# Kernel optimization log

Hardware: AMD Instinct MI355X
Metric: run time of the kernel (lower is better)

## Reference

```python
import jax, jax.numpy as jnp
import numpy as np

N = 150000   # total supergraph nodes (entities+events+chains)
D = 128      # embed_size
H = 4        # attention heads
DH = D // H  # head dim
E = 300000   # edges per layer
L = 4        # layer_specs length
A = 8        # edge attr dim
T = 10       # num_edge_type
TIME_SCALE = 24.0
SLOPE = 0.2  # negative_slope


def setup_inputs() -> dict:
    key = jax.random.key(0)
    ks = jax.random.split(key, 16)
    nrm = lambda k, s, sc=1.0: jax.random.normal(k, s, dtype=jnp.float32) * sc
    return {
        'x': nrm(ks[0], (N, D), 0.1),
        'Wq': nrm(ks[1], (L, D, D), D ** -0.5),
        'Wk': nrm(ks[2], (L, D, D), D ** -0.5),
        'Wv': nrm(ks[3], (L, D, D), D ** -0.5),
        'Wskip': nrm(ks[4], (L, D, D), D ** -0.5),
        'Wa': nrm(ks[5], (L, A, D), 0.1),
        'time_w': nrm(ks[6], (D,)),
        'time_b': nrm(ks[7], (D,), 0.1),
        'dist_w': nrm(ks[8], (D,)),
        'dist_b': nrm(ks[9], (D,), 0.1),
        'type_table': nrm(ks[10], (T, D), 0.1),
        'bn_gamma': jnp.ones((L, D), jnp.float32),
        'bn_beta': jnp.zeros((L, D), jnp.float32),
        'beta': jnp.full((L,), 0.5, jnp.float32),
        'edge_attr': jax.random.uniform(ks[11], (L, E, A), dtype=jnp.float32),
        'edge_dt': jax.random.uniform(ks[12], (L, E), dtype=jnp.float32) * TIME_SCALE,
        'edge_ds': jax.random.uniform(ks[13], (L, E), dtype=jnp.float32) * 10.0,
        'edge_index': jax.random.randint(ks[14], (L, 2, E), 0, N),
        'edge_type': jax.random.randint(ks[15], (L, E), 0, T),
    }


def _layer(x, Wq, Wk, Wv, Wskip, Wa, time_w, time_b, dist_w, dist_b,
           type_table, gamma, bvec, beta, attr, dt, ds, ei, et):
    n = x.shape[0]
    src, dst = ei[0], ei[1]
    # continuous time / distance encoders: cos basis (TimeEncoder / 'time' DistanceEncoder)
    te = jnp.cos((dt / TIME_SCALE)[:, None] * time_w + time_b)   # [E,D]
    de = jnp.cos(ds[:, None] * dist_w + dist_b)                  # [E,D]
    # 'add' edge/time fusion: attr MLP + time + dist + edge-type embeddings
    edge_feat = attr @ Wa + te + de + type_table[et]             # [E,D]
    kv_in = x[src] + edge_feat                                   # gather + fuse
    q = (x @ Wq).reshape(n, H, DH)[dst]                          # [E,H,DH]
    k = (kv_in @ Wk).reshape(-1, H, DH)
    v = (kv_in @ Wv).reshape(-1, H, DH)
    logits = (q * k).sum(-1) * (DH ** -0.5)                      # [E,H]
    logits = jnp.where(logits >= 0, logits, SLOPE * logits)      # leaky_relu(negative_slope)
    # segment softmax over incoming edges of each destination node
    m = jax.ops.segment_max(logits, dst, num_segments=n)
    a = jnp.exp(logits - m[dst])
    denom = jax.ops.segment_sum(a, dst, num_segments=n)
    a = a / denom[dst]
    agg = jax.ops.segment_sum(a[..., None] * v, dst, num_segments=n).reshape(n, D)
    # beta-weighted residual (learn_beta) with skip projection
    out = beta * (x @ Wskip) + (1.0 - beta) * agg
    # BatchNorm1d (training-mode batch stats) + ReLU
    mu = out.mean(0)
    var = out.var(0)
    out = (out - mu) * jax.lax.rsqrt(var + 1e-5) * gamma + bvec
    return jax.nn.relu(out)


def reference(x, Wq, Wk, Wv, Wskip, Wa, time_w, time_b, dist_w, dist_b,
              type_table, bn_gamma, bn_beta, beta, edge_attr, edge_dt,
              edge_ds, edge_index, edge_type):
    for l in range(L):  # entity2event, event2event, event2chain (time filter), chain2chain
        x = _layer(x, Wq[l], Wk[l], Wv[l], Wskip[l], Wa[l],
                   time_w, time_b, dist_w, dist_b, type_table,
                   bn_gamma[l], bn_beta[l], beta[l],
                   edge_attr[l], edge_dt[l], edge_ds[l],
                   edge_index[l], edge_type[l])
    return x
```

## Files before the change

kernel.cpp:

```cpp
#include <hip/hip_runtime.h>

typedef unsigned int u32;
typedef unsigned short u16;
typedef short bf16x8 __attribute__((ext_vector_type(8)));
typedef float f32x4 __attribute__((ext_vector_type(4)));

#define N_NODES 150000
#define E_EDGES 300000
#define L_CNT   151552
#define ETILES  9375
#define NTILES  4688

__device__ __forceinline__ float blo(u32 u){ return __uint_as_float(u << 16); }
__device__ __forceinline__ float bhi(u32 u){ return __uint_as_float(u & 0xffff0000u); }
__device__ __forceinline__ float b2f(u16 h){ return __uint_as_float(((u32)h) << 16); }
__device__ __forceinline__ u16 f2bf(float f){
  u32 u = __float_as_uint(f);
  return (u16)((u + 0x7fffu + ((u >> 16) & 1u)) >> 16);
}
__device__ __forceinline__ u32 pack2(float a, float b){
  return (u32)f2bf(a) | ((u32)f2bf(b) << 16);
}

__device__ __forceinline__ f32x4 mfma16(bf16x8 a, bf16x8 b, f32x4 c){
  return __builtin_amdgcn_mfma_f32_16x16x32_bf16(a, b, c, 0, 0, 0);
}

__device__ __forceinline__ int opsw(int r, int k){ return (r * 128 + k) ^ ((r & 7) << 3); }
__device__ __forceinline__ int csw(int r, int n){ return (r * 128 + n) ^ (((r >> 2) & 3) << 3); }

__global__ __launch_bounds__(256)
void k_wt(const float* __restrict__ Wq, const float* __restrict__ Wk,
          const float* __restrict__ Wv, const float* __restrict__ Ws,
          u16* __restrict__ Wt)
{
  const int m = blockIdx.x;
  const float* src = (m < 4 ? Wq : m < 8 ? Wk : m < 12 ? Wv : Ws)
                     + (size_t)(m & 3) * 16384;
  u16* dst = Wt + (size_t)m * 16384;
  const int t = threadIdx.x;
  for (int i = 0; i < 16; ++i) {
    int idx = i * 256 + t;
    int n = idx >> 5;
    int k4 = (idx & 31) << 2;
    ushort4 o;
    o.x = f2bf(src[(k4 + 0) * 128 + n]);
    o.y = f2bf(src[(k4 + 1) * 128 + n]);
    o.z = f2bf(src[(k4 + 2) * 128 + n]);
    o.w = f2bf(src[(k4 + 3) * 128 + n]);
    *(ushort4*)(dst + n * 128 + k4) = o;
  }
}


__global__ __launch_bounds__(256)
void k_hist(const int* __restrict__ eidx, int* __restrict__ counts)
{
  const int l = blockIdx.y;
  const int e = blockIdx.x * 256 + threadIdx.x;
  if (e < E_EDGES) {
    int dst = eidx[(size_t)l * 2 * E_EDGES + E_EDGES + e];
    atomicAdd(&counts[(size_t)l * L_CNT + dst], 1);
  }
}

__global__ __launch_bounds__(256)
void k_scan1(const int* __restrict__ counts, int* __restrict__ rowptr,
             int* __restrict__ bsum)
{
  __shared__ int sh[256];
  const int b = blockIdx.x, l = blockIdx.y;
  const int t = threadIdx.x;
  const int* c = counts + (size_t)l * L_CNT + b * 2048;
  int* rp = rowptr + (size_t)l * L_CNT + b * 2048;
  int v[8]; int s = 0;
  #pragma unroll
  for (int j = 0; j < 8; ++j) { v[j] = c[t * 8 + j]; s += v[j]; }
  sh[t] = s; __syncthreads();
  for (int off = 1; off < 256; off <<= 1) {
    int x = (t >= off) ? sh[t - off] : 0;
    __syncthreads();
    sh[t] += x;
    __syncthreads();
  }
  int excl = (t == 0) ? 0 : sh[t - 1];
  if (t == 255) bsum[l * 128 + b] = sh[255];
  int run = excl;
  #pragma unroll
  for (int j = 0; j < 8; ++j) { rp[t * 8 + j] = run; run += v[j]; }
}

__global__ __launch_bounds__(128)
void k_scan2(int* __restrict__ bsum)
{
  __shared__ int sh[128];
  const int l = blockIdx.x, t = threadIdx.x;
  int v = (t < 74) ? bsum[l * 128 + t] : 0;
  sh[t] = v; __syncthreads();
  for (int off = 1; off < 128; off <<= 1) {
    int x = (t >= off) ? sh[t - off] : 0;
    __syncthreads();
    sh[t] += x;
    __syncthreads();
  }
  int excl = (t == 0) ? 0 : sh[t - 1];
  if (t < 74) bsum[l * 128 + t] = excl;
}

__global__ __launch_bounds__(256)
void k_scan3(int* __restrict__ rowptr, int* __restrict__ tmp,
             const int* __restrict__ bsum)
{
  const int l = blockIdx.y;
  const int q = blockIdx.x * 256 + threadIdx.x;
  int v = rowptr[(size_t)l * L_CNT + q] + bsum[l * 128 + (q >> 11)];
  rowptr[(size_t)l * L_CNT + q] = v;
  tmp[(size_t)l * L_CNT + q] = v;
}

__global__ __launch_bounds__(256)
void k_scatter(const int* __restrict__ srcP, const int* __restrict__ dstP,
               const int* __restrict__ etP, const float* __restrict__ dtP,
               const float* __restrict__ dsP, const float* __restrict__ attrP,
               int* __restrict__ tmpL, u32* __restrict__ meta)
{
  const int e = blockIdx.x * 256 + threadIdx.x;
  if (e < E_EDGES) {
    int dst = dstP[e];
    int pos = atomicAdd(&tmpL[dst], 1);
    int src = srcP[e];
    int et  = etP[e];
    float dtn = dtP[e] * (1.0f / 24.0f);
    float dsv = dsP[e];
    float4 aA = *(const float4*)(attrP + (size_t)e * 8);
    float4 aB = *(const float4*)(attrP + (size_t)e * 8 + 4);
    uint4 r0, r1;
    r0.x = (u32)src;
    r0.y = (u32)dst | ((u32)et << 20);
    r0.z = __float_as_uint(dtn);
    r0.w = __float_as_uint(dsv);
    r1.x = pack2(aA.x, aA.y); r1.y = pack2(aA.z, aA.w);
    r1.z = pack2(aB.x, aB.y); r1.w = pack2(aB.z, aB.w);
    u32* mp = meta + (size_t)pos * 8;
    *(uint4*)mp = r0;
    *(uint4*)(mp + 4) = r1;
  }
}

template<int XF32>
__global__ __launch_bounds__(256)
void k_kvin(const void* __restrict__ xg, const float* __restrict__ Wa,
            const float* __restrict__ tw, const float* __restrict__ tb,
            const float* __restrict__ dw, const float* __restrict__ db,
            const float* __restrict__ ttab, const u32* __restrict__ meta,
            u16* __restrict__ kvV)
{
  const int idx = blockIdx.x * 256 + threadIdx.x;
  const int e = idx >> 4;
  const int c8 = (idx & 15) << 3;
  const u32* mp = meta + (size_t)e * 8;
  uint4 m0 = *(const uint4*)mp;
  uint4 m1 = *(const uint4*)(mp + 4);
  const int src = (int)m0.x;
  const int et = (int)(m0.y >> 20);
  const float dtn = __uint_as_float(m0.z);
  const float dss = __uint_as_float(m0.w);
  float aa[8] = { blo(m1.x), bhi(m1.x), blo(m1.y), bhi(m1.y),
                  blo(m1.z), bhi(m1.z), blo(m1.w), bhi(m1.w) };
  const float4 twA = *(const float4*)(tw + c8);
  const float4 twB = *(const float4*)(tw + c8 + 4);
  const float4 tbA = *(const float4*)(tb + c8);
  const float4 tbB = *(const float4*)(tb + c8 + 4);
  const float4 dwA = *(const float4*)(dw + c8);
  const float4 dwB = *(const float4*)(dw + c8 + 4);
  const float4 dbA = *(const float4*)(db + c8);
  const float4 dbB = *(const float4*)(db + c8 + 4);
  const float4 ttA = *(const float4*)(ttab + et * 128 + c8);
  const float4 ttB = *(const float4*)(ttab + et * 128 + c8 + 4);
  float f[8];
  f[0] = __cosf(fmaf(dtn, twA.x, tbA.x)) + __cosf(fmaf(dss, dwA.x, dbA.x)) + ttA.x;
  f[1] = __cosf(fmaf(dtn, twA.y, tbA.y)) + __cosf(fmaf(dss, dwA.y, dbA.y)) + ttA.y;
  f[2] = __cosf(fmaf(dtn, twA.z, tbA.z)) + __cosf(fmaf(dss, dwA.z, dbA.z)) + ttA.z;
  f[3] = __cosf(fmaf(dtn, twA.w, tbA.w)) + __cosf(fmaf(dss, dwA.w, dbA.w)) + ttA.w;
  f[4] = __cosf(fmaf(dtn, twB.x, tbB.x)) + __cosf(fmaf(dss, dwB.x, dbB.x)) + ttB.x;
  f[5] = __cosf(fmaf(dtn, twB.y, tbB.y)) + __cosf(fmaf(dss, dwB.y, dbB.y)) + ttB.y;
  f[6] = __cosf(fmaf(dtn, twB.z, tbB.z)) + __cosf(fmaf(dss, dwB.z, dbB.z)) + ttB.z;
  f[7] = __cosf(fmaf(dtn, twB.w, tbB.w)) + __cosf(fmaf(dss, dwB.w, dbB.w)) + ttB.w;
  #pragma unroll
  for (int a = 0; a < 8; ++a) {
    float4 wA = *(const float4*)(Wa + a * 128 + c8);
    float4 wB = *(const float4*)(Wa + a * 128 + c8 + 4);
    f[0] = fmaf(aa[a], wA.x, f[0]);
    f[1] = fmaf(aa[a], wA.y, f[1]);
    f[2] = fmaf(aa[a], wA.z, f[2]);
    f[3] = fmaf(aa[a], wA.w, f[3]);
    f[4] = fmaf(aa[a], wB.x, f[4]);
    f[5] = fmaf(aa[a], wB.y, f[5]);
    f[6] = fmaf(aa[a], wB.z, f[6]);
    f[7] = fmaf(aa[a], wB.w, f[7]);
  }
  float xv[8];
  if (XF32) {
    float4 xA = *(const float4*)((const float*)xg + (size_t)src * 128 + c8);
    float4 xB = *(const float4*)((const float*)xg + (size_t)src * 128 + c8 + 4);
    xv[0] = xA.x; xv[1] = xA.y; xv[2] = xA.z; xv[3] = xA.w;
    xv[4] = xB.x; xv[5] = xB.y; xv[6] = xB.z; xv[7] = xB.w;
  } else {
    uint4 xr = *(const uint4*)((const u16*)xg + (size_t)src * 128 + c8);
    xv[0] = blo(xr.x); xv[1] = bhi(xr.x); xv[2] = blo(xr.y); xv[3] = bhi(xr.y);
    xv[4] = blo(xr.z); xv[5] = bhi(xr.z); xv[6] = blo(xr.w); xv[7] = bhi(xr.w);
  }
  uint4 o;
  o.x = pack2(xv[0] + f[0], xv[1] + f[1]);
  o.y = pack2(xv[2] + f[2], xv[3] + f[3]);
  o.z = pack2(xv[4] + f[4], xv[5] + f[5]);
  o.w = pack2(xv[6] + f[6], xv[7] + f[7]);
  *(uint4*)(kvV + (size_t)e * 128 + c8) = o;
}

template<int XF32>
__global__ __launch_bounds__(64, 2)
void gemm_qs(const void* __restrict__ xg, const u16* __restrict__ WtQ,
             const u16* __restrict__ WtS, u16* __restrict__ Qo,
             u16* __restrict__ So)
{
  __shared__ __align__(16) u16 As[4160];
  const u16* Wt = blockIdx.y ? WtS : WtQ;
  u16* C = blockIdx.y ? So : Qo;
  const int lane = threadIdx.x;
  const int lr = lane & 15, hi = lane >> 4;

  bf16x8 wt[8][4];
  #pragma unroll
  for (int nb = 0; nb < 8; ++nb)
    #pragma unroll
    for (int ks = 0; ks < 4; ++ks)
      wt[nb][ks] = *(const bf16x8*)(Wt + (nb * 16 + lr) * 128 + ks * 32 + hi * 8);

  for (int tile = blockIdx.x; tile < NTILES; tile += gridDim.x) {
    const int row0 = tile * 32;
    const int nr = min(32, N_NODES - row0);

    #pragma unroll
    for (int i = 0; i < 8; ++i) {
      int idx = i * 64 + lane;
      int r = idx >> 4, c8 = (idx & 15) << 3;
      if (r < nr) {
        if (XF32) {
          float4 vA = *(const float4*)((const float*)xg + (size_t)(row0 + r) * 128 + c8);
          float4 vB = *(const float4*)((const float*)xg + (size_t)(row0 + r) * 128 + c8 + 4);
          uint4 o;
          o.x = pack2(vA.x, vA.y); o.y = pack2(vA.z, vA.w);
          o.z = pack2(vB.x, vB.y); o.w = pack2(vB.z, vB.w);
          *(uint4*)(As + opsw(r, c8)) = o;
        } else {
          uint4 v = *(const uint4*)((const u16*)xg + (size_t)(row0 + r) * 128 + c8);
          *(uint4*)(As + opsw(r, c8)) = v;
        }
      } else {
        *(uint4*)(As + opsw(r, c8)) = make_uint4(0, 0, 0, 0);
      }
    }

    f32x4 acc[2][8];
    #pragma unroll
    for (int a = 0; a < 2; ++a)
      #pragma unroll
      for (int b = 0; b < 8; ++b) {
        acc[a][b][0] = 0.f; acc[a][b][1] = 0.f;
        acc[a][b][2] = 0.f; acc[a][b][3] = 0.f;
      }
    #pragma unroll
    for (int ks = 0; ks < 4; ++ks) {
      const int kb = ks * 32 + hi * 8;
      bf16x8 a0 = *(const bf16x8*)(As + opsw(lr, kb));
      bf16x8 a1 = *(const bf16x8*)(As + opsw(16 + lr, kb));
      #pragma unroll
      for (int nb = 0; nb < 8; ++nb) {
        acc[0][nb] = mfma16(a0, wt[nb][ks], acc[0][nb]);
        acc[1][nb] = mfma16(a1, wt[nb][ks], acc[1][nb]);
      }
    }
    const int g4 = hi << 2;
    #pragma unroll
    for (int mt = 0; mt < 2; ++mt)
      #pragma unroll
      for (int nt = 0; nt < 8; ++nt)
        #pragma unroll
        for (int j = 0; j < 4; ++j)
          As[csw(mt * 16 + g4 + j, nt * 16 + lr)] = f2bf(acc[mt][nt][j]);
    #pragma unroll
    for (int i = 0; i < 8; ++i) {
      int idx = i * 64 + lane;
      int r = idx >> 4, n8 = (idx & 15) << 3;
      if (r < nr) {
        uint4 v = *(const uint4*)(As + csw(r, n8));
        *(uint4*)(C + (size_t)(row0 + r) * 128 + n8) = v;
      }
    }
  }
}

__global__ __launch_bounds__(64, 2)
void edge_k(const u16* __restrict__ WtK, const u32* __restrict__ meta,
            const u16* __restrict__ Qb, const u16* __restrict__ kvV,
            float* __restrict__ logits)
{
  __shared__ __align__(16) u16 As[4160];
  __shared__ __align__(16) u16 Qs[4160];
  __shared__ int dstSh[32];
  const int lane = threadIdx.x;
  const int lr = lane & 15, hi = lane >> 4;

  bf16x8 wt[8][4];
  #pragma unroll
  for (int nb = 0; nb < 8; ++nb)
    #pragma unroll
    for (int ks = 0; ks < 4; ++ks)
      wt[nb][ks] = *(const bf16x8*)(WtK + (nb * 16 + lr) * 128 + ks * 32 + hi * 8);

  for (int tile = blockIdx.x; tile < ETILES; tile += gridDim.x) {
    const int e0 = tile * 32;
    if (lane < 32)
      dstSh[lane] = (int)(meta[(size_t)(e0 + lane) * 8 + 1] & 0xFFFFFu);

    #pragma unroll
    for (int i = 0; i < 8; ++i) {
      int idx = i * 64 + lane;
      int r = idx >> 4, c8 = (idx & 15) << 3;
      uint4 v = *(const uint4*)(kvV + (size_t)(e0 + r) * 128 + c8);
      *(uint4*)(As + opsw(r, c8)) = v;
      int qrow = dstSh[r];
      uint4 qv = *(const uint4*)(Qb + (size_t)qrow * 128 + c8);
      *(uint4*)(Qs + opsw(r, c8)) = qv;
    }

    #pragma unroll
    for (int eb = 0; eb < 2; ++eb) {
      f32x4 kacc[8];
      #pragma unroll
      for (int b = 0; b < 8; ++b) {
        kacc[b][0] = 0.f; kacc[b][1] = 0.f; kacc[b][2] = 0.f; kacc[b][3] = 0.f;
      }
      #pragma unroll
      for (int ks = 0; ks < 4; ++ks) {
        bf16x8 ef = *(const bf16x8*)(As + opsw(eb * 16 + lr, ks * 32 + hi * 8));
        #pragma unroll
        for (int nb = 0; nb < 8; ++nb)
          kacc[nb] = mfma16(wt[nb][ks], ef, kacc[nb]);
      }
      const int el = eb * 16 + lr;
      float hs[4] = {0.f, 0.f, 0.f, 0.f};
      #pragma unroll
      for (int nb = 0; nb < 8; ++nb) {
        ushort4 q = *(const ushort4*)(Qs + opsw(el, nb * 16 + hi * 4));
        hs[nb >> 1] += b2f(q.x) * kacc[nb][0] + b2f(q.y) * kacc[nb][1]
                     + b2f(q.z) * kacc[nb][2] + b2f(q.w) * kacc[nb][3];
      }
      #pragma unroll
      for (int h = 0; h < 4; ++h) {
        hs[h] += __shfl_xor(hs[h], 16, 64);
        hs[h] += __shfl_xor(hs[h], 32, 64);
        hs[h] *= 0.17677669529663687f;
        hs[h] = (hs[h] >= 0.f) ? hs[h] : 0.2f * hs[h];
      }
      if (lane < 16)
        *(float4*)(logits + (size_t)(e0 + el) * 4) = make_float4(hs[0], hs[1], hs[2], hs[3]);
    }
  }
}

__global__ __launch_bounds__(64, 2)
void edge_v(const u16* __restrict__ WtV, u16* __restrict__ kvV)
{
  __shared__ __align__(16) u16 As[4160];
  const int lane = threadIdx.x;
  const int lr = lane & 15, hi = lane >> 4;

  bf16x8 wt[8][4];
  #pragma unroll
  for (int nb = 0; nb < 8; ++nb)
    #pragma unroll
    for (int ks = 0; ks < 4; ++ks)
      wt[nb][ks] = *(const bf16x8*)(WtV + (nb * 16 + lr) * 128 + ks * 32 + hi * 8);

  for (int tile = blockIdx.x; tile < ETILES; tile += gridDim.x) {
    const int e0 = tile * 32;
    #pragma unroll
    for (int i = 0; i < 8; ++i) {
      int idx = i * 64 + lane;
      int r = idx >> 4, c8 = (idx & 15) << 3;
      uint4 v = *(const uint4*)(kvV + (size_t)(e0 + r) * 128 + c8);
      *(uint4*)(As + opsw(r, c8)) = v;
    }
    const int g4 = hi << 2;
    #pragma unroll
    for (int mt = 0; mt < 2; ++mt) {
      f32x4 vacc[8];
      #pragma unroll
      for (int b = 0; b < 8; ++b) {
        vacc[b][0] = 0.f; vacc[b][1] = 0.f; vacc[b][2] = 0.f; vacc[b][3] = 0.f;
      }
      #pragma unroll
      for (int ks = 0; ks < 4; ++ks) {
        bf16x8 af = *(const bf16x8*)(As + opsw(mt * 16 + lr, ks * 32 + hi * 8));
        #pragma unroll
        for (int nb = 0; nb < 8; ++nb)
          vacc[nb] = mfma16(af, wt[nb][ks], vacc[nb]);
      }
      #pragma unroll
      for (int nt = 0; nt < 8; ++nt)
        #pragma unroll
        for (int j = 0; j < 4; ++j)
          As[csw(mt * 16 + g4 + j, nt * 16 + lr)] = f2bf(vacc[nt][j]);
    }
    #pragma unroll
    for (int i = 0; i < 8; ++i) {
      int idx = i * 64 + lane;
      int r = idx >> 4, n8 = (idx & 15) << 3;
      uint4 v = *(const uint4*)(As + csw(r, n8));
      *(uint4*)(kvV + (size_t)(e0 + r) * 128 + n8) = v;
    }
  }
}

__global__ __launch_bounds__(256)
void node_agg(const u16* __restrict__ Vs, const float* __restrict__ logits,
              const int* __restrict__ rowptr, const u16* __restrict__ S,
              const float* __restrict__ betaP, float* __restrict__ pre,
              float* __restrict__ colsum, float* __restrict__ colsumsq)
{
  __shared__ float red[1024];
  const int t = threadIdx.x;
  const int g = t >> 5;
  const int lane = t & 31;
  const int d0 = lane * 4;
  const int h = lane >> 3;
  const float beta = *betaP;
  const float omb = 1.f - beta;
  float s4[4] = {0.f, 0.f, 0.f, 0.f};
  float q4[4] = {0.f, 0.f, 0.f, 0.f};
  for (int rep = 0; rep < 16; ++rep) {
    int n = blockIdx.x * 128 + rep * 8 + g;
    if (n < N_NODES) {
      int rs = rowptr[n], re = rowptr[n + 1];
      float m = -1e30f;
      for (int i = rs; i < re; ++i)
        m = fmaxf(m, logits[(size_t)i * 4 + h]);
      float den = 0.f;
      float a0 = 0.f, a1 = 0.f, a2 = 0.f, a3 = 0.f;
      for (int i = rs; i < re; ++i) {
        float wgt = __expf(logits[(size_t)i * 4 + h] - m);
        den += wgt;
        ushort4 v = *(const ushort4*)(Vs + (size_t)i * 128 + d0);
        a0 = fmaf(wgt, b2f(v.x), a0);
        a1 = fmaf(wgt, b2f(v.y), a1);
        a2 = fmaf(wgt, b2f(v.z), a2);
        a3 = fmaf(wgt, b2f(v.w), a3);
      }
      float inv = (den > 0.f) ? (omb / den) : 0.f;
      ushort4 sv = *(const ushort4*)(S + (size_t)n * 128 + d0);
      float p0 = fmaf(beta, b2f(sv.x), a0 * inv);
      float p1 = fmaf(beta, b2f(sv.y), a1 * inv);
      float p2 = fmaf(beta, b2f(sv.z), a2 * inv);
      float p3 = fmaf(beta, b2f(sv.w), a3 * inv);
      *(float4*)(pre + (size_t)n * 128 + d0) = make_float4(p0, p1, p2, p3);
      s4[0] += p0; s4[1] += p1; s4[2] += p2; s4[3] += p3;
      q4[0] += p0 * p0; q4[1] += p1 * p1; q4[2] += p2 * p2; q4[3] += p3 * p3;
    }
  }
  *(float4*)(&red[g * 128 + d0]) = make_float4(s4[0], s4[1], s4[2], s4[3]);
  __syncthreads();
  if (t < 128) {
    float tot = 0.f;
    #pragma unroll
    for (int gg = 0; gg < 8; ++gg) tot += red[gg * 128 + t];
    atomicAdd(&colsum[t], tot);
  }
  __syncthreads();
  *(float4*)(&red[g * 128 + d0]) = make_float4(q4[0], q4[1], q4[2], q4[3]);
  __syncthreads();
  if (t < 128) {
    float tot = 0.f;
    #pragma unroll
    for (int gg = 0; gg < 8; ++gg) tot += red[gg * 128 + t];
    atomicAdd(&colsumsq[t], tot);
  }
}

template<int LAST>
__global__ __launch_bounds__(256)
void bn_apply(const float* __restrict__ pre, const float* __restrict__ colsum,
              const float* __restrict__ colsumsq, const float* __restrict__ gamma,
              const float* __restrict__ bvec, u16* __restrict__ outbf,
              float* __restrict__ outf)
{
  const int idx = blockIdx.x * 256 + threadIdx.x;
  const int n = idx >> 5;
  const int d0 = (idx & 31) * 4;
  const float invN = 1.f / 150000.f;
  float4 p = *(const float4*)(pre + (size_t)n * 128 + d0);
  float4 cs = *(const float4*)(colsum + d0);
  float4 cq = *(const float4*)(colsumsq + d0);
  float4 gm = *(const float4*)(gamma + d0);
  float4 bv = *(const float4*)(bvec + d0);
  float mu, var, y;
  mu = cs.x * invN; var = cq.x * invN - mu * mu;
  y = (p.x - mu) * rsqrtf(var + 1e-5f) * gm.x + bv.x; p.x = fmaxf(y, 0.f);
  mu = cs.y * invN; var = cq.y * invN - mu * mu;
  y = (p.y - mu) * rsqrtf(var + 1e-5f) * gm.y + bv.y; p.y = fmaxf(y, 0.f);
  mu = cs.z * invN; var = cq.z * invN - mu * mu;
  y = (p.z - mu) * rsqrtf(var + 1e-5f) * gm.z + bv.z; p.z = fmaxf(y, 0.f);
  mu = cs.w * invN; var = cq.w * invN - mu * mu;
  y = (p.w - mu) * rsqrtf(var + 1e-5f) * gm.w + bv.w; p.w = fmaxf(y, 0.f);
  if (LAST) {
    *(float4*)(outf + (size_t)n * 128 + d0) = p;
  } else {
    ushort4 o;
    o.x = f2bf(p.x); o.y = f2bf(p.y); o.z = f2bf(p.z); o.w = f2bf(p.w);
    *(ushort4*)(outbf + (size_t)n * 128 + d0) = o;
  }
}

extern "C" void kernel_launch(void* const* d_in, const int* in_sizes, int n_in,
                              void* d_out, int out_size, void* d_ws, size_t ws_size,
                              hipStream_t stream)
{
  const float* x0    = (const float*)d_in[0];
  const float* Wq    = (const float*)d_in[1];
  const float* Wk    = (const float*)d_in[2];
  const float* Wv    = (const float*)d_in[3];
  const float* Wsk   = (const float*)d_in[4];
  const float* Wa    = (const float*)d_in[5];
  const float* tw    = (const float*)d_in[6];
  const float* tb    = (const float*)d_in[7];
  const float* dw    = (const float*)d_in[8];
  const float* db    = (const float*)d_in[9];
  const float* ttab  = (const float*)d_in[10];
  const float* gam   = (const float*)d_in[11];
  const float* bet   = (const float*)d_in[12];
  const float* betaP = (const float*)d_in[13];
  const float* attr  = (const float*)d_in[14];
  const float* dt    = (const float*)d_in[15];
  const float* dsv   = (const float*)d_in[16];
  const int*   eidx  = (const int*)d_in[17];
  const int*   etyp  = (const int*)d_in[18];

  char* p = (char*)d_ws;
  u16* xbf  = (u16*)p;       p += 38400000;
  u16* Q    = (u16*)p;       p += 38400000;
  u16* S    = (u16*)p;       p += 38400000;
  u16* kvV  = (u16*)p;       p += 76800000;
  float* logits = (float*)p; p += 4800000;
  int* rowptr = (int*)p;     p += 4 * L_CNT * 4;
  int* tmp    = (int*)p;     p += 4 * L_CNT * 4;
  int* bsum   = (int*)p;     p += 4 * 128 * 4;
  float* colsum   = (float*)p; p += 512;
  float* colsumsq = (float*)p; p += 512;
  u16* Wt = (u16*)p;         p += 16 * 16384 * 2;
  u32* meta = (u32*)p;       p += (size_t)E_EDGES * 32;

  float* pre = (float*)d_out;

  k_wt<<<16, 256, 0, stream>>>(Wq, Wk, Wv, Wsk, Wt);
  hipMemsetAsync(tmp, 0, 4 * L_CNT * 4, stream);
  k_hist<<<dim3(1172, 4), 256, 0, stream>>>(eidx, tmp);
  k_scan1<<<dim3(74, 4), 256, 0, stream>>>(tmp, rowptr, bsum);
  k_scan2<<<4, 128, 0, stream>>>(bsum);
  k_scan3<<<dim3(592, 4), 256, 0, stream>>>(rowptr, tmp, bsum);

  for (int l = 0; l < 4; ++l) {
    const int* srcA = eidx + (size_t)l * 600000;
    const int* dstA = srcA + 300000;
    const int* rpl = rowptr + (size_t)l * L_CNT;
    const u16* WtQl = Wt + (size_t)l * 16384;
    const u16* WtKl = Wt + (size_t)(4 + l) * 16384;
    const u16* WtVl = Wt + (size_t)(8 + l) * 16384;
    const u16* WtSl = Wt + (size_t)(12 + l) * 16384;
    const float* Wal = Wa + (size_t)l * 1024;

    k_scatter<<<1172, 256, 0, stream>>>(
        srcA, dstA, etyp + (size_t)l * 300000, dt + (size_t)l * 300000,
        dsv + (size_t)l * 300000, attr + (size_t)l * 2400000,
        tmp + (size_t)l * L_CNT, meta);

    hipMemsetAsync(colsum, 0, 1024, stream);

    if (l == 0) {
      k_kvin<1><<<18750, 256, 0, stream>>>((const void*)x0, Wal, tw, tb, dw, db,
                                           ttab, meta, kvV);
      gemm_qs<1><<<dim3(1024, 2), 64, 0, stream>>>((const void*)x0, WtQl, WtSl, Q, S);
    } else {
      k_kvin<0><<<18750, 256, 0, stream>>>((const void*)xbf, Wal, tw, tb, dw, db,
                                           ttab, meta, kvV);
      gemm_qs<0><<<dim3(1024, 2), 64, 0, stream>>>((const void*)xbf, WtQl, WtSl, Q, S);
    }

    edge_k<<<2048, 64, 0, stream>>>(WtKl, meta, Q, kvV, logits);
    edge_v<<<2048, 64, 0, stream>>>(WtVl, kvV);

    node_agg<<<1172, 256, 0, stream>>>(kvV, logits, rpl, S, betaP + l,
                                       pre, colsum, colsumsq);

    if (l < 3)
      bn_apply<0><<<18750, 256, 0, stream>>>(pre, colsum, colsumsq,
                                             gam + (size_t)l * 128,
                                             bet + (size_t)l * 128, xbf, nullptr);
    else
      bn_apply<1><<<18750, 256, 0, stream>>>(pre, colsum, colsumsq,
                                             gam + (size_t)l * 128,
                                             bet + (size_t)l * 128,
                                             nullptr, (float*)d_out);
  }
}
```

Baseline: 1.587 ms.

## Fuse edge K and V projections into one kernel, share staged tiles across waves

Merges the separate edge_k and edge_v kernels into a single two-wave kernel. One wave computes the K projection and attention logits, the other computes the V projection from the same shared-memory tile of kv_in, so kvV is read once instead of twice and one launch is saved. gemm_qs likewise uses one block of two waves (Q and skip) that shares a single staged x tile, so x is read once rather than by two separate blocks. Both kernels drop their grid-stride persistent loops in favour of one tile per block, which means every block reloads its weight fragments into registers and so adds weight-load traffic.

```diff
diff --git a/kernel.cpp b/kernel.cpp
--- a/kernel.cpp
+++ b/kernel.cpp
@@ -218,17 +218,22 @@
   *(uint4*)(kvV + (size_t)e * 128 + c8) = o;
 }
 
+
 template<int XF32>
-__global__ __launch_bounds__(64, 2)
+__global__ __launch_bounds__(128, 2)
 void gemm_qs(const void* __restrict__ xg, const u16* __restrict__ WtQ,
              const u16* __restrict__ WtS, u16* __restrict__ Qo,
              u16* __restrict__ So)
 {
   __shared__ __align__(16) u16 As[4160];
-  const u16* Wt = blockIdx.y ? WtS : WtQ;
-  u16* C = blockIdx.y ? So : Qo;
-  const int lane = threadIdx.x;
+  __shared__ __align__(16) u16 Bs[4160];
+  const int t = threadIdx.x;
+  const int w = t >> 6, lane = t & 63;
   const int lr = lane & 15, hi = lane >> 4;
+  const int row0 = blockIdx.x * 32;
+  const int nr = min(32, N_NODES - row0);
+  const u16* Wt = w ? WtS : WtQ;
+  u16* C = w ? So : Qo;
 
   bf16x8 wt[8][4];
   #pragma unroll
@@ -237,104 +242,115 @@
     for (int ks = 0; ks < 4; ++ks)
       wt[nb][ks] = *(const bf16x8*)(Wt + (nb * 16 + lr) * 128 + ks * 32 + hi * 8);
 
-  for (int tile = blockIdx.x; tile < NTILES; tile += gridDim.x) {
-    const int row0 = tile * 32;
-    const int nr = min(32, N_NODES - row0);
-
+  #pragma unroll
+  for (int i = 0; i < 4; ++i) {
+    int idx = i * 128 + t;
+    int r = idx >> 4, c8 = (idx & 15) << 3;
+    if (r < nr) {
+      if (XF32) {
+        float4 vA = *(const float4*)((const float*)xg + (size_t)(row0 + r) * 128 + c8);
+        float4 vB = *(const float4*)((const float*)xg + (size_t)(row0 + r) * 128 + c8 + 4);
+        uint4 o;
+        o.x = pack2(vA.x, vA.y); o.y = pack2(vA.z, vA.w);
+        o.z = pack2(vB.x, vB.y); o.w = pack2(vB.z, vB.w);
+        *(uint4*)(As + opsw(r, c8)) = o;
+      } else {
+        uint4 v = *(const uint4*)((const u16*)xg + (size_t)(row0 + r) * 128 + c8);
+        *(uint4*)(As + opsw(r, c8)) = v;
+      }
+    } else {
+      *(uint4*)(As + opsw(r, c8)) = make_uint4(0, 0, 0, 0);
+    }
+  }
+  __syncthreads();
+
+  f32x4 acc[2][8];
+  #pragma unroll
+  for (int a = 0; a < 2; ++a)
+    #pragma unroll
+    for (int b = 0; b < 8; ++b) {
+      acc[a][b][0] = 0.f; acc[a][b][1] = 0.f;
+      acc[a][b][2] = 0.f; acc[a][b][3] = 0.f;
+    }
+  #pragma unroll
+  for (int ks = 0; ks < 4; ++ks) {
+    const int kb = ks * 32 + hi * 8;
+    bf16x8 a0 = *(const bf16x8*)(As + opsw(lr, kb));
+    bf16x8 a1 = *(const bf16x8*)(As + opsw(16 + lr, kb));
+    #pragma unroll
+    for (int nb = 0; nb < 8; ++nb) {
+      acc[0][nb] = mfma16(a0, wt[nb][ks], acc[0][nb]);
+      acc[1][nb] = mfma16(a1, wt[nb][ks], acc[1][nb]);
+    }
+  }
+  __syncthreads();
+
+  u16* Cs = w ? Bs : As;
+  const int g4 = hi << 2;
+  #pragma unroll
+  for (int mt = 0; mt < 2; ++mt)
+    #pragma unroll
+    for (int nt = 0; nt < 8; ++nt)
+      #pragma unroll
+      for (int j = 0; j < 4; ++j)
+        Cs[csw(mt * 16 + g4 + j, nt * 16 + lr)] = f2bf(acc[mt][nt][j]);
+  #pragma unroll
+  for (int i = 0; i < 8; ++i) {
+    int idx = i * 64 + lane;
+    int r = idx >> 4, n8 = (idx & 15) << 3;
+    if (r < nr) {
+      uint4 v = *(const uint4*)(Cs + csw(r, n8));
+      *(uint4*)(C + (size_t)(row0 + r) * 128 + n8) = v;
+    }
+  }
+}
+
+
+__global__ __launch_bounds__(128, 2)
+void edge_kv(const u16* __restrict__ WtK, const u16* __restrict__ WtV,
+             const u32* __restrict__ meta, const u16* __restrict__ Qb,
+             u16* __restrict__ kvV, float* __restrict__ logits)
+{
+  __shared__ __align__(16) u16 KVs[4160];
+  __shared__ __align__(16) u16 Qs[4160];
+  __shared__ __align__(16) u16 Cs[4160];
+  __shared__ int dstSh[32];
+  const int t = threadIdx.x;
+  const int w = t >> 6, lane = t & 63;
+  const int lr = lane & 15, hi = lane >> 4;
+  const int e0 = blockIdx.x * 32;
+  const u16* Wt = w ? WtV : WtK;
+
+  bf16x8 wt[8][4];
+  #pragma unroll
+  for (int nb = 0; nb < 8; ++nb)
+    #pragma unroll
+    for (int ks = 0; ks < 4; ++ks)
+      wt[nb][ks] = *(const bf16x8*)(Wt + (nb * 16 + lr) * 128 + ks * 32 + hi * 8);
+
+  if (t < 32)
+    dstSh[t] = (int)(meta[(size_t)(e0 + t) * 8 + 1] & 0xFFFFFu);
+
+  #pragma unroll
+  for (int i = 0; i < 4; ++i) {
+    int idx = i * 128 + t;
+    int r = idx >> 4, c8 = (idx & 15) << 3;
+    uint4 v = *(const uint4*)(kvV + (size_t)(e0 + r) * 128 + c8);
+    *(uint4*)(KVs + opsw(r, c8)) = v;
+  }
+  if (w == 0) {
     #pragma unroll
     for (int i = 0; i < 8; ++i) {
       int idx = i * 64 + lane;
       int r = idx >> 4, c8 = (idx & 15) << 3;
-      if (r < nr) {
-        if (XF32) {
-          float4 vA = *(const float4*)((const float*)xg + (size_t)(row0 + r) * 128 + c8);
-          float4 vB = *(const float4*)((const float*)xg + (size_t)(row0 + r) * 128 + c8 + 4);
-          uint4 o;
-          o.x = pack2(vA.x, vA.y); o.y = pack2(vA.z, vA.w);
-          o.z = pack2(vB.x, vB.y); o.w = pack2(vB.z, vB.w);
-          *(uint4*)(As + opsw(r, c8)) = o;
-        } else {
-          uint4 v = *(const uint4*)((const u16*)xg + (size_t)(row0 + r) * 128 + c8);
-          *(uint4*)(As + opsw(r, c8)) = v;
-        }
-      } else {
-        *(uint4*)(As + opsw(r, c8)) = make_uint4(0, 0, 0, 0);
-      }
-    }
-
-    f32x4 acc[2][8];
-    #pragma unroll
-    for (int a = 0; a < 2; ++a)
-      #pragma unroll
-      for (int b = 0; b < 8; ++b) {
-        acc[a][b][0] = 0.f; acc[a][b][1] = 0.f;
-        acc[a][b][2] = 0.f; acc[a][b][3] = 0.f;
-      }
-    #pragma unroll
-    for (int ks = 0; ks < 4; ++ks) {
-      const int kb = ks * 32 + hi * 8;
-      bf16x8 a0 = *(const bf16x8*)(As + opsw(lr, kb));
-      bf16x8 a1 = *(const bf16x8*)(As + opsw(16 + lr, kb));
-      #pragma unroll
-      for (int nb = 0; nb < 8; ++nb) {
-        acc[0][nb] = mfma16(a0, wt[nb][ks], acc[0][nb]);
-        acc[1][nb] = mfma16(a1, wt[nb][ks], acc[1][nb]);
-      }
-    }
-    const int g4 = hi << 2;
-    #pragma unroll
-    for (int mt = 0; mt < 2; ++mt)
-      #pragma unroll
-      for (int nt = 0; nt < 8; ++nt)
-        #pragma unroll
-        for (int j = 0; j < 4; ++j)
-          As[csw(mt * 16 + g4 + j, nt * 16 + lr)] = f2bf(acc[mt][nt][j]);
-    #pragma unroll
-    for (int i = 0; i < 8; ++i) {
-      int idx = i * 64 + lane;
-      int r = idx >> 4, n8 = (idx & 15) << 3;
-      if (r < nr) {
-        uint4 v = *(const uint4*)(As + csw(r, n8));
-        *(uint4*)(C + (size_t)(row0 + r) * 128 + n8) = v;
-      }
-    }
-  }
-}
-
-__global__ __launch_bounds__(64, 2)
-void edge_k(const u16* __restrict__ WtK, const u32* __restrict__ meta,
-            const u16* __restrict__ Qb, const u16* __restrict__ kvV,
-            float* __restrict__ logits)
-{
-  __shared__ __align__(16) u16 As[4160];
-  __shared__ __align__(16) u16 Qs[4160];
-  __shared__ int dstSh[32];
-  const int lane = threadIdx.x;
-  const int lr = lane & 15, hi = lane >> 4;
-
-  bf16x8 wt[8][4];
-  #pragma unroll
-  for (int nb = 0; nb < 8; ++nb)
-    #pragma unroll
-    for (int ks = 0; ks < 4; ++ks)
-      wt[nb][ks] = *(const bf16x8*)(WtK + (nb * 16 + lr) * 128 + ks * 32 + hi * 8);
-
-  for (int tile = blockIdx.x; tile < ETILES; tile += gridDim.x) {
-    const int e0 = tile * 32;
-    if (lane < 32)
-      dstSh[lane] = (int)(meta[(size_t)(e0 + lane) * 8 + 1] & 0xFFFFFu);
-
-    #pragma unroll
-    for (int i = 0; i < 8; ++i) {
-      int idx = i * 64 + lane;
-      int r = idx >> 4, c8 = (idx & 15) << 3;
-      uint4 v = *(const uint4*)(kvV + (size_t)(e0 + r) * 128 + c8);
-      *(uint4*)(As + opsw(r, c8)) = v;
       int qrow = dstSh[r];
       uint4 qv = *(const uint4*)(Qb + (size_t)qrow * 128 + c8);
       *(uint4*)(Qs + opsw(r, c8)) = qv;
     }
-
+  }
+  __syncthreads();
+
+  if (w == 0) {
     #pragma unroll
     for (int eb = 0; eb < 2; ++eb) {
       f32x4 kacc[8];
@@ -344,7 +360,7 @@
       }
       #pragma unroll
       for (int ks = 0; ks < 4; ++ks) {
-        bf16x8 ef = *(const bf16x8*)(As + opsw(eb * 16 + lr, ks * 32 + hi * 8));
+        bf16x8 ef = *(const bf16x8*)(KVs + opsw(eb * 16 + lr, ks * 32 + hi * 8));
         #pragma unroll
         for (int nb = 0; nb < 8; ++nb)
           kacc[nb] = mfma16(wt[nb][ks], ef, kacc[nb]);
@@ -367,32 +383,7 @@
       if (lane < 16)
         *(float4*)(logits + (size_t)(e0 + el) * 4) = make_float4(hs[0], hs[1], hs[2], hs[3]);
     }
-  }
-}
-
-__global__ __launch_bounds__(64, 2)
-void edge_v(const u16* __restrict__ WtV, u16* __restrict__ kvV)
-{
-  __shared__ __align__(16) u16 As[4160];
-  const int lane = threadIdx.x;
-  const int lr = lane & 15, hi = lane >> 4;
-
-  bf16x8 wt[8][4];
-  #pragma unroll
-  for (int nb = 0; nb < 8; ++nb)
-    #pragma unroll
-    for (int ks = 0; ks < 4; ++ks)
-      wt[nb][ks] = *(const bf16x8*)(WtV + (nb * 16 + lr) * 128 + ks * 32 + hi * 8);
-
-  for (int tile = blockIdx.x; tile < ETILES; tile += gridDim.x) {
-    const int e0 = tile * 32;
-    #pragma unroll
-    for (int i = 0; i < 8; ++i) {
-      int idx = i * 64 + lane;
-      int r = idx >> 4, c8 = (idx & 15) << 3;
-      uint4 v = *(const uint4*)(kvV + (size_t)(e0 + r) * 128 + c8);
-      *(uint4*)(As + opsw(r, c8)) = v;
-    }
+  } else {
     const int g4 = hi << 2;
     #pragma unroll
     for (int mt = 0; mt < 2; ++mt) {
@@ -403,7 +394,7 @@
       }
       #pragma unroll
       for (int ks = 0; ks < 4; ++ks) {
-        bf16x8 af = *(const bf16x8*)(As + opsw(mt * 16 + lr, ks * 32 + hi * 8));
+        bf16x8 af = *(const bf16x8*)(KVs + opsw(mt * 16 + lr, ks * 32 + hi * 8));
         #pragma unroll
         for (int nb = 0; nb < 8; ++nb)
           vacc[nb] = mfma16(af, wt[nb][ks], vacc[nb]);
@@ -412,13 +403,13 @@
       for (int nt = 0; nt < 8; ++nt)
         #pragma unroll
         for (int j = 0; j < 4; ++j)
-          As[csw(mt * 16 + g4 + j, nt * 16 + lr)] = f2bf(vacc[nt][j]);
+          Cs[csw(mt * 16 + g4 + j, nt * 16 + lr)] = f2bf(vacc[nt][j]);
     }
     #pragma unroll
     for (int i = 0; i < 8; ++i) {
       int idx = i * 64 + lane;
       int r = idx >> 4, n8 = (idx & 15) << 3;
-      uint4 v = *(const uint4*)(As + csw(r, n8));
+      uint4 v = *(const uint4*)(Cs + csw(r, n8));
       *(uint4*)(kvV + (size_t)(e0 + r) * 128 + n8) = v;
     }
   }
@@ -589,15 +580,14 @@
     if (l == 0) {
       k_kvin<1><<<18750, 256, 0, stream>>>((const void*)x0, Wal, tw, tb, dw, db,
                                            ttab, meta, kvV);
-      gemm_qs<1><<<dim3(1024, 2), 64, 0, stream>>>((const void*)x0, WtQl, WtSl, Q, S);
+      gemm_qs<1><<<NTILES, 128, 0, stream>>>((const void*)x0, WtQl, WtSl, Q, S);
     } else {
       k_kvin<0><<<18750, 256, 0, stream>>>((const void*)xbf, Wal, tw, tb, dw, db,
                                            ttab, meta, kvV);
-      gemm_qs<0><<<dim3(1024, 2), 64, 0, stream>>>((const void*)xbf, WtQl, WtSl, Q, S);
-    }
-
-    edge_k<<<2048, 64, 0, stream>>>(WtKl, meta, Q, kvV, logits);
-    edge_v<<<2048, 64, 0, stream>>>(WtVl, kvV);
+      gemm_qs<0><<<NTILES, 128, 0, stream>>>((const void*)xbf, WtQl, WtSl, Q, S);
+    }
+
+    edge_kv<<<ETILES, 128, 0, stream>>>(WtKl, WtVl, meta, Q, kvV, logits);
 
     node_agg<<<1172, 256, 0, stream>>>(kvV, logits, rpl, S, betaP + l,
                                        pre, colsum, colsumsq);
```

New measurement: 1.495 ms. -5.8%, faster.
